# Kernel tuning notes

Measured on AMD Instinct MI355X. Metric: run time of the kernel, lower is better.

## Reference

```python
import jax, jax.numpy as jnp
import numpy as np

N, FDIM, HDIM, STEPS = 8192, 512, 1024, 50
STRESS, QNOISE = 0.0, 0.1


def setup_inputs() -> dict:
    key = jax.random.key(0)
    ks = jax.random.split(key, 20)
    s = 0.02
    d = {
        "real_antigen": jax.random.normal(ks[0], (N, FDIM), jnp.float32),
        "steps": STEPS,
        # quantum gene projection (self-loop graph -> per-node linear)
        "Wq": jax.random.normal(ks[1], (FDIM, HDIM), jnp.float32) * s,
        "bq": jnp.zeros((HDIM,), jnp.float32),
        # denoise_0: Linear(h,h) ReLU Linear(h,f)
        "W01": jax.random.normal(ks[2], (HDIM, HDIM), jnp.float32) * s,
        "b01": jnp.zeros((HDIM,), jnp.float32),
        "W02": jax.random.normal(ks[3], (HDIM, FDIM), jnp.float32) * s,
        "b02": jnp.zeros((FDIM,), jnp.float32),
        # denoise_1: Linear(h,h) Tanh Linear(h,f)
        "W11": jax.random.normal(ks[4], (HDIM, HDIM), jnp.float32) * s,
        "b11": jnp.zeros((HDIM,), jnp.float32),
        "W12": jax.random.normal(ks[5], (HDIM, FDIM), jnp.float32) * s,
        "b12": jnp.zeros((FDIM,), jnp.float32),
        # interference_net: Linear(2f,h) GELU Linear(h,f)
        "Wi1": jax.random.normal(ks[6], (2 * FDIM, HDIM), jnp.float32) * s,
        "bi1": jnp.zeros((HDIM,), jnp.float32),
        "Wi2": jax.random.normal(ks[7], (HDIM, FDIM), jnp.float32) * s,
        "bi2": jnp.zeros((FDIM,), jnp.float32),
        # quantum state scalars
        "alpha_amp": jnp.asarray(np.cos(0.6), jnp.float32),
        "beta_amp": jnp.asarray(np.sin(0.6), jnp.float32),
        "phase_cos": jnp.asarray(np.cos(0.3), jnp.float32),
    }
    return d


def reference(real_antigen, steps, Wq, bq, W01, b01, W02, b02, W11, b11,
              W12, b12, Wi1, bi1, Wi2, bi2, alpha_amp, beta_amp, phase_cos):
    sched = jnp.linspace(1e-4, 0.02, 100, dtype=jnp.float32)
    decoherence_rate = jnp.float32(0.1 + STRESS * 0.5)
    decay = jnp.exp(-decoherence_rate)
    # quantum probabilities (fixed amplitudes during the rollout)
    a2, b2 = alpha_amp ** 2, beta_amp ** 2
    p0 = a2 / (a2 + b2)
    p1 = b2 / (a2 + b2)
    sp0, sp1 = jnp.sqrt(p0), jnp.sqrt(p1)
    base_key = jax.random.key(1)
    x0 = jax.random.normal(jax.random.fold_in(base_key, 10_000), real_antigen.shape, jnp.float32)

    def step(carry, t):
        x, coh = carry
        qf = jax.nn.relu(x @ Wq + bq)                           # [N, H]
        d0 = jax.nn.relu(qf @ W01 + b01) @ W02 + b02            # [N, F]
        d1 = jnp.tanh(qf @ W11 + b11) @ W12 + b12               # [N, F]
        inter_in = jnp.concatenate([d0, d1], axis=-1)           # [N, 2F]
        interf = jax.nn.gelu(inter_in @ Wi1 + bi1, approximate=False) @ Wi2 + bi2
        qi = 2.0 * jnp.sqrt(p0 * p1) * phase_cos * coh          # scalar interference
        denoised = sp0 * d0 + sp1 * d1 + qi * interf
        alpha = jnp.maximum(1.0 - sched[t], 1e-8)
        alpha_prev = jnp.where(t > 0, 1.0 - sched[jnp.maximum(t - 1, 0)], 1.0)
        sqrt_1ma = jnp.sqrt(jnp.maximum(1.0 - alpha, 1e-8))
        x_new = (x - (1.0 - alpha) / sqrt_1ma * denoised) / jnp.sqrt(alpha)
        sigma = jnp.sqrt(jnp.maximum((1.0 - alpha_prev) / (1.0 - alpha) * (1.0 - alpha / alpha_prev), 0.0))
        noise = jax.random.normal(jax.random.fold_in(base_key, t), x.shape, jnp.float32)
        x_new = jnp.where(t > 0, x_new + (sigma + QNOISE * jnp.abs(qi)) * noise, x_new)
        return (x_new, coh * decay), None

    ts = jnp.arange(int(steps) - 1, -1, -1, dtype=jnp.int32)
    (x, _), _ = jax.lax.scan(step, (x0, jnp.float32(1.0)), ts)
    # quantum measurement: collapse to |0> with probability p0
    u = jax.random.uniform(jax.random.fold_in(base_key, 99_999), (), jnp.float32)
    dream = jnp.where(u < p0, 0.7 * x + 0.3 * real_antigen, x)
    return dream
```

## Files before the change

kernel.cpp:

```cpp
#include <hip/hip_runtime.h>
#include <stdint.h>
#include <math.h>


typedef __bf16 bf16x8 __attribute__((ext_vector_type(8)));
typedef float floatx4 __attribute__((ext_vector_type(4)));

__host__ __device__ inline void tf2x32(uint32_t k0, uint32_t k1,
                                       uint32_t x0, uint32_t x1,
                                       uint32_t& o0, uint32_t& o1) {
  uint32_t ks2 = k0 ^ k1 ^ 0x1BD11BDAu;
#define TF_R(r) { x0 += x1; x1 = (x1 << (r)) | (x1 >> (32 - (r))); x1 ^= x0; }
  x0 += k0; x1 += k1;
  TF_R(13) TF_R(15) TF_R(26) TF_R(6)
  x0 += k1;  x1 += ks2 + 1u;
  TF_R(17) TF_R(29) TF_R(16) TF_R(24)
  x0 += ks2; x1 += k0 + 2u;
  TF_R(13) TF_R(15) TF_R(26) TF_R(6)
  x0 += k0;  x1 += k1 + 3u;
  TF_R(17) TF_R(29) TF_R(16) TF_R(24)
  x0 += k1;  x1 += ks2 + 4u;
  TF_R(13) TF_R(15) TF_R(26) TF_R(6)
  x0 += ks2; x1 += k0 + 5u;
#undef TF_R
  o0 = x0; o1 = x1;
}

__device__ inline float erfinv_f32(float x) {
  float w = -log1pf(-x * x);
  float p;
  if (w < 5.0f) {
    w = w - 2.5f;
    p = 2.81022636e-08f;
    p = fmaf(p, w, 3.43273939e-07f);
    p = fmaf(p, w, -3.5233877e-06f);
    p = fmaf(p, w, -4.39150654e-06f);
    p = fmaf(p, w, 0.00021858087f);
    p = fmaf(p, w, -0.00125372503f);
    p = fmaf(p, w, -0.00417768164f);
    p = fmaf(p, w, 0.246640727f);
    p = fmaf(p, w, 1.50140941f);
  } else {
    w = sqrtf(w) - 3.0f;
    p = -0.000200214257f;
    p = fmaf(p, w, 0.000100950558f);
    p = fmaf(p, w, 0.00134934322f);
    p = fmaf(p, w, -0.00367342844f);
    p = fmaf(p, w, 0.00573950773f);
    p = fmaf(p, w, -0.0076224613f);
    p = fmaf(p, w, 0.00943887047f);
    p = fmaf(p, w, 1.00167406f);
    p = fmaf(p, w, 2.83297682f);
  }
  return p * x;
}

__device__ inline float tf_normal(uint32_t k0, uint32_t k1, uint32_t i) {
  uint32_t o0, o1;
  tf2x32(k0, k1, 0u, i, o0, o1);
  uint32_t bits = o0 ^ o1;
  float f = __uint_as_float(0x3F800000u | (bits >> 9)) - 1.0f;
  float u = f * 2.0f + (-0.99999994f);
  u = fmaxf(-0.99999994f, u);
  return 1.41421356f * erfinv_f32(u);
}

__device__ inline unsigned short f2bf(float f) {
  uint32_t u = __float_as_uint(f);
  u += 0x7FFFu + ((u >> 16) & 1u);
  return (unsigned short)(u >> 16);
}
__device__ inline float bf2f(unsigned short h) {
  return __uint_as_float(((uint32_t)h) << 16);
}

__global__ __launch_bounds__(256)
void transpose_bf16_kernel(const float* __restrict__ W,
                           unsigned short* __restrict__ Wt, int K, int N) {
  __shared__ float tile[32][33];
  int kb = blockIdx.x * 32, nb = blockIdx.y * 32;
  int tx = threadIdx.x & 31, ty = threadIdx.x >> 5;
#pragma unroll
  for (int i = 0; i < 32; i += 8)
    tile[ty + i][tx] = W[(size_t)(kb + ty + i) * N + nb + tx];
  __syncthreads();
#pragma unroll
  for (int i = 0; i < 32; i += 8)
    Wt[(size_t)(nb + ty + i) * K + kb + tx] = f2bf(tile[tx][ty + i]);
}

__device__ __forceinline__ void gemm_core_db(
    const unsigned short* __restrict__ A0, const unsigned short* __restrict__ A1,
    int lda0, int lda1, int K0, int Ktot,
    const unsigned short* __restrict__ Bt,
    int row0, int col0,
    unsigned short (*As)[128 * 32], unsigned short (*Bs)[128 * 32],
    floatx4 (&acc)[2][4]) {
  const int tid = threadIdx.x;
  const int wave = tid >> 6, lane = tid & 63;
  const int wr = wave >> 1, wc = wave & 1;
  const int srow = tid >> 2;
  const int sgr = (tid & 3) * 8;
  const int fm = lane & 15, quad = lane >> 4;

  auto issue = [&](int kt, int buf) {
    const int k0 = kt * 32;
    const unsigned short* Ap; int kOff, lda;
    if (k0 < K0) { Ap = A0; kOff = k0; lda = lda0; }
    else         { Ap = A1; kOff = k0 - K0; lda = lda1; }
    __builtin_amdgcn_global_load_lds(
        (const __attribute__((address_space(1))) uint32_t*)
            (Ap + (size_t)(row0 + srow) * lda + kOff + sgr),
        (__attribute__((address_space(3))) uint32_t*)(&As[buf][srow * 32 + sgr]),
        16, 0, 0);
    __builtin_amdgcn_global_load_lds(
        (const __attribute__((address_space(1))) uint32_t*)
            (Bt + (size_t)(col0 + srow) * Ktot + k0 + sgr),
        (__attribute__((address_space(3))) uint32_t*)(&Bs[buf][srow * 32 + sgr]),
        16, 0, 0);
  };

  const int nk = Ktot >> 5;
  issue(0, 0);
  for (int k = 0; k < nk; k++) {
    const int cur = k & 1;
    if (k + 1 < nk) {
      issue(k + 1, cur ^ 1);
      asm volatile("s_waitcnt vmcnt(2)\ns_barrier" ::: "memory");
    } else {
      asm volatile("s_waitcnt vmcnt(0)\ns_barrier" ::: "memory");
    }
    bf16x8 a[2], b[4];
#pragma unroll
    for (int tm = 0; tm < 2; tm++)
      a[tm] = *(const bf16x8*)(&As[cur][(wr * 32 + tm * 16 + fm) * 32 + quad * 8]);
#pragma unroll
    for (int tn = 0; tn < 4; tn++)
      b[tn] = *(const bf16x8*)(&Bs[cur][(wc * 64 + tn * 16 + fm) * 32 + quad * 8]);
#pragma unroll
    for (int tm = 0; tm < 2; tm++)
#pragma unroll
      for (int tn = 0; tn < 4; tn++)
        acc[tm][tn] = __builtin_amdgcn_mfma_f32_16x16x32_bf16(a[tm], b[tn],
                                                              acc[tm][tn], 0, 0, 0);
    asm volatile("s_barrier" ::: "memory");
  }
}

__device__ __forceinline__ void swizzled_block(int& row0, int& col0) {
  int id = blockIdx.x + gridDim.x * blockIdx.y;
  row0 = (id & 63) << 7;
  col0 = (id >> 6) << 7;
}

template<int ACT>
__global__ __launch_bounds__(512, 4)
void mfma_gemm(const unsigned short* __restrict__ A0,
               const unsigned short* __restrict__ A1,
               int lda0, int lda1, int K0, int Ktot,
               const unsigned short* __restrict__ Bt,
               const float* __restrict__ bias0,
               const float* __restrict__ bias1, int nsplit,
               unsigned short* __restrict__ C0,
               unsigned short* __restrict__ C1, int ldc) {
  __shared__ unsigned short As[2][128 * 32];
  __shared__ unsigned short Bs[2][128 * 32];
  int row0, col0;
  swizzled_block(row0, col0);
  floatx4 acc[2][4];
#pragma unroll
  for (int tm = 0; tm < 2; tm++)
#pragma unroll
    for (int tn = 0; tn < 4; tn++) acc[tm][tn] = (floatx4){0.f, 0.f, 0.f, 0.f};
  gemm_core_db(A0, A1, lda0, lda1, K0, Ktot, Bt, row0, col0, As, Bs, acc);

  const int lane = threadIdx.x & 63, wave = threadIdx.x >> 6;
  const int wr = wave >> 1, wc = wave & 1;
  const int fm = lane & 15, quad = lane >> 4;
  const bool side = (ACT == 4) && (col0 >= nsplit);
  const float* bias = side ? bias1 : bias0;
  unsigned short* C = side ? C1 : C0;
  const int cbase = col0 - (side ? nsplit : 0);
#pragma unroll
  for (int tn = 0; tn < 4; tn++) {
    int col = cbase + wc * 64 + tn * 16 + fm;
    float bv = bias[col];
#pragma unroll
    for (int tm = 0; tm < 2; tm++) {
      int rbase = row0 + wr * 32 + tm * 16 + quad * 4;
#pragma unroll
      for (int r = 0; r < 4; r++) {
        float val = acc[tm][tn][r] + bv;
        if (ACT == 1) val = fmaxf(val, 0.0f);
        if (ACT == 2) val = tanhf(val);
        if (ACT == 3) val = 0.5f * val * (1.0f + erff(val * 0.70710678118654752f));
        if (ACT == 4) val = side ? tanhf(val) : fmaxf(val, 0.0f);
        C[(size_t)(rbase + r) * ldc + col] = f2bf(val);
      }
    }
  }
}

__global__ __launch_bounds__(512, 4)
void mfma_gemm_pair(const unsigned short* __restrict__ Aa,
                    const unsigned short* __restrict__ Ab,
                    const unsigned short* __restrict__ Bta,
                    const unsigned short* __restrict__ Btb,
                    const float* __restrict__ biasa,
                    const float* __restrict__ biasb,
                    unsigned short* __restrict__ Ca,
                    unsigned short* __restrict__ Cb,
                    int Ktot, int ldc) {
  __shared__ unsigned short As[2][128 * 32];
  __shared__ unsigned short Bs[2][128 * 32];
  const int z = blockIdx.z;
  const unsigned short* A = z ? Ab : Aa;
  const unsigned short* Bt = z ? Btb : Bta;
  const float* bias = z ? biasb : biasa;
  unsigned short* C = z ? Cb : Ca;
  int row0, col0;
  swizzled_block(row0, col0);
  floatx4 acc[2][4];
#pragma unroll
  for (int tm = 0; tm < 2; tm++)
#pragma unroll
    for (int tn = 0; tn < 4; tn++) acc[tm][tn] = (floatx4){0.f, 0.f, 0.f, 0.f};
  gemm_core_db(A, A, Ktot, Ktot, Ktot, Ktot, Bt, row0, col0, As, Bs, acc);

  const int lane = threadIdx.x & 63, wave = threadIdx.x >> 6;
  const int wr = wave >> 1, wc = wave & 1;
  const int fm = lane & 15, quad = lane >> 4;
#pragma unroll
  for (int tn = 0; tn < 4; tn++) {
    int col = col0 + wc * 64 + tn * 16 + fm;
    float bv = bias[col];
#pragma unroll
    for (int tm = 0; tm < 2; tm++) {
      int rbase = row0 + wr * 32 + tm * 16 + quad * 4;
#pragma unroll
      for (int r = 0; r < 4; r++)
        C[(size_t)(rbase + r) * ldc + col] = f2bf(acc[tm][tn][r] + bv);
    }
  }
}

__global__ void init_normal_kernel(float* __restrict__ x,
                                   unsigned short* __restrict__ xbf,
                                   uint32_t k0, uint32_t k1, int n) {
  int i = blockIdx.x * blockDim.x + threadIdx.x;
  if (i >= n) return;
  float v = tf_normal(k0, k1, (uint32_t)i);
  x[i] = v;
  xbf[i] = f2bf(v);
}

__global__ void update_kernel(float* __restrict__ x,
                              unsigned short* __restrict__ xbf,
                              const unsigned short* __restrict__ d0,
                              const unsigned short* __restrict__ d1,
                              const unsigned short* __restrict__ itf,
                              const float* __restrict__ a_amp,
                              const float* __restrict__ b_amp,
                              const float* __restrict__ ph,
                              float coh, float c1, float sqrt_alpha,
                              float sigma, int add_noise,
                              uint32_t k0, uint32_t k1, int n) {
  int i = blockIdx.x * blockDim.x + threadIdx.x;
  if (i >= n) return;
  float aa = a_amp[0], bb = b_amp[0], pc = ph[0];
  float a2 = aa * aa, b2 = bb * bb, s = a2 + b2;
  float p0 = a2 / s, p1 = b2 / s;
  float qi = 2.0f * sqrtf(p0 * p1) * pc * coh;
  float den = sqrtf(p0) * bf2f(d0[i]) + sqrtf(p1) * bf2f(d1[i])
            + qi * bf2f(itf[i]);
  float xn = (x[i] - c1 * den) / sqrt_alpha;
  if (add_noise) {
    float nz = tf_normal(k0, k1, (uint32_t)i);
    xn += (sigma + 0.1f * fabsf(qi)) * nz;
  }
  x[i] = xn;
  xbf[i] = f2bf(xn);
}

__global__ void final_kernel(const float* __restrict__ x,
                             const float* __restrict__ real,
                             float* __restrict__ out,
                             const float* __restrict__ a_amp,
                             const float* __restrict__ b_amp,
                             uint32_t k0, uint32_t k1, int n) {
  int i = blockIdx.x * blockDim.x + threadIdx.x;
  if (i >= n) return;
  float aa = a_amp[0], bb = b_amp[0];
  float a2 = aa * aa, b2 = bb * bb;
  float p0 = a2 / (a2 + b2);
  uint32_t o0, o1;
  tf2x32(k0, k1, 0u, 0u, o0, o1);
  uint32_t bits = o0 ^ o1;
  float u = __uint_as_float(0x3F800000u | (bits >> 9)) - 1.0f;
  float xv = x[i];
  out[i] = (u < p0) ? (0.7f * xv + 0.3f * real[i]) : xv;
}

extern "C" void kernel_launch(void* const* d_in, const int* in_sizes, int n_in,
                              void* d_out, int out_size, void* d_ws,
                              size_t ws_size, hipStream_t stream) {
  const float* real = (const float*)d_in[0];
  const float* Wq  = (const float*)d_in[2];
  const float* bq  = (const float*)d_in[3];
  const float* W01 = (const float*)d_in[4];
  const float* b01 = (const float*)d_in[5];
  const float* W02 = (const float*)d_in[6];
  const float* b02 = (const float*)d_in[7];
  const float* W11 = (const float*)d_in[8];
  const float* b11 = (const float*)d_in[9];
  const float* W12 = (const float*)d_in[10];
  const float* b12 = (const float*)d_in[11];
  const float* Wi1 = (const float*)d_in[12];
  const float* bi1 = (const float*)d_in[13];
  const float* Wi2 = (const float*)d_in[14];
  const float* bi2 = (const float*)d_in[15];
  const float* a_amp = (const float*)d_in[16];
  const float* b_amp = (const float*)d_in[17];
  const float* ph    = (const float*)d_in[18];

  const int Nn = 8192, F = 512, H = 1024;
  const int nElem = Nn * F;
  const int NSPLIT_OFF = 1 << 30;

  char* ws = (char*)d_ws;
  float* x = (float*)ws;                                   ws += (size_t)nElem * 4;
  unsigned short* xbf = (unsigned short*)ws;               ws += (size_t)nElem * 2;
  unsigned short* qf  = (unsigned short*)ws;               ws += (size_t)Nn * H * 2;
  unsigned short* h0  = (unsigned short*)ws;               ws += (size_t)Nn * H * 2;
  unsigned short* h1  = (unsigned short*)ws;               ws += (size_t)Nn * H * 2;
  unsigned short* d0  = (unsigned short*)ws;               ws += (size_t)nElem * 2;
  unsigned short* d1  = (unsigned short*)ws;               ws += (size_t)nElem * 2;
  unsigned short* itf = (unsigned short*)ws;               ws += (size_t)nElem * 2;
  unsigned short* Wq_t  = (unsigned short*)ws;             ws += (size_t)F * H * 2;
  unsigned short* WA_t  = (unsigned short*)ws;             ws += (size_t)(2 * H) * H * 2;
  unsigned short* W02_t = (unsigned short*)ws;             ws += (size_t)H * F * 2;
  unsigned short* W12_t = (unsigned short*)ws;             ws += (size_t)H * F * 2;
  unsigned short* Wi1_t = (unsigned short*)ws;             ws += (size_t)(2 * F) * H * 2;
  unsigned short* Wi2_t = (unsigned short*)ws;             ws += (size_t)H * F * 2;

  dim3 tb(256);
  transpose_bf16_kernel<<<dim3(F / 32, H / 32), tb, 0, stream>>>(Wq, Wq_t, F, H);
  transpose_bf16_kernel<<<dim3(H / 32, H / 32), tb, 0, stream>>>(W01, WA_t, H, H);
  transpose_bf16_kernel<<<dim3(H / 32, H / 32), tb, 0, stream>>>(W11, WA_t + (size_t)H * H, H, H);
  transpose_bf16_kernel<<<dim3(H / 32, F / 32), tb, 0, stream>>>(W02, W02_t, H, F);
  transpose_bf16_kernel<<<dim3(H / 32, F / 32), tb, 0, stream>>>(W12, W12_t, H, F);
  transpose_bf16_kernel<<<dim3(2 * F / 32, H / 32), tb, 0, stream>>>(Wi1, Wi1_t, 2 * F, H);
  transpose_bf16_kernel<<<dim3(H / 32, F / 32), tb, 0, stream>>>(Wi2, Wi2_t, H, F);

  uint32_t kx0, kx1; tf2x32(0u, 1u, 0u, 10000u, kx0, kx1);
  init_normal_kernel<<<(nElem + 255) / 256, 256, 0, stream>>>(x, xbf, kx0, kx1, nElem);

  float sched[100];
  for (int i = 0; i < 100; i++)
    sched[i] = (float)(1e-4 + (0.02 - 1e-4) * (double)i / 99.0);
  const float decay = expf(-0.1f);
  float coh = 1.0f;

  dim3 blk(512);
  dim3 g1(H / 128, 64);
  dim3 g2(2 * H / 128, 64);
  dim3 g45(F / 128, 64, 2);
  dim3 g6(H / 128, 64);
  dim3 g7(F / 128, 64);

  for (int j = 0; j < 50; j++) {
    int t = 49 - j;
    mfma_gemm<1><<<g1, blk, 0, stream>>>(xbf, xbf, F, F, F, F, Wq_t,
                                         bq, nullptr, NSPLIT_OFF, qf, nullptr, H);
    mfma_gemm<4><<<g2, blk, 0, stream>>>(qf, qf, H, H, H, H, WA_t,
                                         b01, b11, H, h0, h1, H);
    mfma_gemm_pair<<<g45, blk, 0, stream>>>(h0, h1, W02_t, W12_t, b02, b12,
                                            d0, d1, H, F);
    mfma_gemm<3><<<g6, blk, 0, stream>>>(d0, d1, F, F, F, 2 * F, Wi1_t,
                                         bi1, nullptr, NSPLIT_OFF, qf, nullptr, H);
    mfma_gemm<0><<<g7, blk, 0, stream>>>(qf, qf, H, H, H, H, Wi2_t,
                                         bi2, nullptr, NSPLIT_OFF, itf, nullptr, F);

    float schedt = sched[t];
    float alphaf = fmaxf(1.0f - schedt, 1e-8f);
    float one_m_alpha = 1.0f - alphaf;
    float sqrt_1ma = sqrtf(fmaxf(one_m_alpha, 1e-8f));
    float c1 = one_m_alpha / sqrt_1ma;
    float sqa = sqrtf(alphaf);
    float sigma = 0.0f;
    if (t > 0) {
      float ap = 1.0f - sched[t - 1];
      sigma = sqrtf(fmaxf((1.0f - ap) / one_m_alpha * (1.0f - alphaf / ap), 0.0f));
    }
    uint32_t kt0, kt1; tf2x32(0u, 1u, 0u, (uint32_t)t, kt0, kt1);
    update_kernel<<<(nElem + 255) / 256, 256, 0, stream>>>(
        x, xbf, d0, d1, itf, a_amp, b_amp, ph, coh, c1, sqa, sigma,
        (t > 0) ? 1 : 0, kt0, kt1, nElem);
    coh *= decay;
  }

  uint32_t ku0, ku1; tf2x32(0u, 1u, 0u, 99999u, ku0, ku1);
  final_kernel<<<(nElem + 255) / 256, 256, 0, stream>>>(
      x, real, (float*)d_out, a_amp, b_amp, ku0, ku1, nElem);
}
```

Baseline: 8.881 ms.

## Fuse interference output GEMM with diffusion update epilogue

Replaces the final Wi2 GEMM plus the separate elementwise update kernel with one MFMA GEMM whose epilogue computes the denoised combination, the noise and the x update directly. This drops the bf16 itf intermediate buffer and one kernel launch per step, saving a write and read of N*F values. The new GEMM uses a smaller 64x128 tile with 8 waves, each doing 2x2 MFMA tiles, and loads into LDS asynchronously via global_load_lds with double buffering. That tiling may lower MFMA efficiency compared with the previous generic GEMM, and the epilogue's scattered per-element loads of x, d0 and d1 may coalesce less well.

```diff
diff --git a/kernel.cpp b/kernel.cpp
--- a/kernel.cpp
+++ b/kernel.cpp
@@ -244,6 +244,107 @@
   }
 }
 
+__global__ __launch_bounds__(512, 4)
+void mfma_gemm_update(const unsigned short* __restrict__ A,
+                      const unsigned short* __restrict__ Bt,
+                      const float* __restrict__ bias,
+                      const unsigned short* __restrict__ d0,
+                      const unsigned short* __restrict__ d1,
+                      float* __restrict__ x,
+                      unsigned short* __restrict__ xbf,
+                      const float* __restrict__ a_amp,
+                      const float* __restrict__ b_amp,
+                      const float* __restrict__ ph,
+                      float coh, float c1, float sqa, float sigma,
+                      int add_noise, uint32_t k0, uint32_t k1) {
+  __shared__ unsigned short As[2][64 * 32];
+  __shared__ unsigned short Bs[2][128 * 32];
+  const int tid = threadIdx.x;
+  const int wave = tid >> 6, lane = tid & 63;
+  const int wr = wave >> 2, wc = wave & 3;
+  const int fm = lane & 15, quad = lane >> 4;
+  const int id = blockIdx.x + gridDim.x * blockIdx.y;
+  const int row0 = (id & 127) << 6;
+  const int col0 = (id >> 7) << 7;
+  const int sArow = (tid & 255) >> 2;
+  const int sBrow = tid >> 2;
+  const int sgr = (tid & 3) * 8;
+
+  auto issue = [&](int kt, int buf) {
+    const int kk = kt * 32;
+    __builtin_amdgcn_global_load_lds(
+        (const __attribute__((address_space(1))) uint32_t*)
+            (A + (size_t)(row0 + sArow) * 1024 + kk + sgr),
+        (__attribute__((address_space(3))) uint32_t*)(&As[buf][sArow * 32 + sgr]),
+        16, 0, 0);
+    __builtin_amdgcn_global_load_lds(
+        (const __attribute__((address_space(1))) uint32_t*)
+            (Bt + (size_t)(col0 + sBrow) * 1024 + kk + sgr),
+        (__attribute__((address_space(3))) uint32_t*)(&Bs[buf][sBrow * 32 + sgr]),
+        16, 0, 0);
+  };
+
+  floatx4 acc[2][2];
+#pragma unroll
+  for (int tm = 0; tm < 2; tm++)
+#pragma unroll
+    for (int tn = 0; tn < 2; tn++) acc[tm][tn] = (floatx4){0.f, 0.f, 0.f, 0.f};
+
+  const int nk = 32;
+  issue(0, 0);
+  for (int k = 0; k < nk; k++) {
+    const int cur = k & 1;
+    if (k + 1 < nk) {
+      issue(k + 1, cur ^ 1);
+      asm volatile("s_waitcnt vmcnt(2)\ns_barrier" ::: "memory");
+    } else {
+      asm volatile("s_waitcnt vmcnt(0)\ns_barrier" ::: "memory");
+    }
+    bf16x8 a[2], b[2];
+#pragma unroll
+    for (int tm = 0; tm < 2; tm++)
+      a[tm] = *(const bf16x8*)(&As[cur][(wr * 32 + tm * 16 + fm) * 32 + quad * 8]);
+#pragma unroll
+    for (int tn = 0; tn < 2; tn++)
+      b[tn] = *(const bf16x8*)(&Bs[cur][(wc * 32 + tn * 16 + fm) * 32 + quad * 8]);
+#pragma unroll
+    for (int tm = 0; tm < 2; tm++)
+#pragma unroll
+      for (int tn = 0; tn < 2; tn++)
+        acc[tm][tn] = __builtin_amdgcn_mfma_f32_16x16x32_bf16(a[tm], b[tn],
+                                                              acc[tm][tn], 0, 0, 0);
+    asm volatile("s_barrier" ::: "memory");
+  }
+
+  float aa = a_amp[0], bb = b_amp[0], pc = ph[0];
+  float a2 = aa * aa, b2 = bb * bb, s = a2 + b2;
+  float p0 = a2 / s, p1 = b2 / s;
+  float sp0 = sqrtf(p0), sp1 = sqrtf(p1);
+  float qi = 2.0f * sqrtf(p0 * p1) * pc * coh;
+  float nscale = sigma + 0.1f * fabsf(qi);
+
+#pragma unroll
+  for (int tn = 0; tn < 2; tn++) {
+    int col = col0 + wc * 32 + tn * 16 + fm;
+    float bv = bias[col];
+#pragma unroll
+    for (int tm = 0; tm < 2; tm++) {
+      int rbase = row0 + wr * 32 + tm * 16 + quad * 4;
+#pragma unroll
+      for (int r = 0; r < 4; r++) {
+        int row = rbase + r;
+        size_t i = (size_t)row * 512 + col;
+        float itf = acc[tm][tn][r] + bv;
+        float den = sp0 * bf2f(d0[i]) + sp1 * bf2f(d1[i]) + qi * itf;
+        float xn = (x[i] - c1 * den) / sqa;
+        if (add_noise) xn += nscale * tf_normal(k0, k1, (uint32_t)i);
+        x[i] = xn;
+        xbf[i] = f2bf(xn);
+      }
+    }
+  }
+}
+
 __global__ void init_normal_kernel(float* __restrict__ x,
                                    unsigned short* __restrict__ xbf,
                                    uint32_t k0, uint32_t k1, int n) {
@@ -252,34 +353,6 @@
   float v = tf_normal(k0, k1, (uint32_t)i);
   x[i] = v;
   xbf[i] = f2bf(v);
-}
-
-__global__ void update_kernel(float* __restrict__ x,
-                              unsigned short* __restrict__ xbf,
-                              const unsigned short* __restrict__ d0,
-                              const unsigned short* __restrict__ d1,
-                              const unsigned short* __restrict__ itf,
-                              const float* __restrict__ a_amp,
-                              const float* __restrict__ b_amp,
-                              const float* __restrict__ ph,
-                              float coh, float c1, float sqrt_alpha,
-                              float sigma, int add_noise,
-                              uint32_t k0, uint32_t k1, int n) {
-  int i = blockIdx.x * blockDim.x + threadIdx.x;
-  if (i >= n) return;
-  float aa = a_amp[0], bb = b_amp[0], pc = ph[0];
-  float a2 = aa * aa, b2 = bb * bb, s = a2 + b2;
-  float p0 = a2 / s, p1 = b2 / s;
-  float qi = 2.0f * sqrtf(p0 * p1) * pc * coh;
-  float den = sqrtf(p0) * bf2f(d0[i]) + sqrtf(p1) * bf2f(d1[i])
-            + qi * bf2f(itf[i]);
-  float xn = (x[i] - c1 * den) / sqrt_alpha;
-  if (add_noise) {
-    float nz = tf_normal(k0, k1, (uint32_t)i);
-    xn += (sigma + 0.1f * fabsf(qi)) * nz;
-  }
-  x[i] = xn;
-  xbf[i] = f2bf(xn);
 }
 
 __global__ void final_kernel(const float* __restrict__ x,
@@ -335,7 +408,6 @@
   unsigned short* h1  = (unsigned short*)ws;               ws += (size_t)Nn * H * 2;
   unsigned short* d0  = (unsigned short*)ws;               ws += (size_t)nElem * 2;
   unsigned short* d1  = (unsigned short*)ws;               ws += (size_t)nElem * 2;
-  unsigned short* itf = (unsigned short*)ws;               ws += (size_t)nElem * 2;
   unsigned short* Wq_t  = (unsigned short*)ws;             ws += (size_t)F * H * 2;
   unsigned short* WA_t  = (unsigned short*)ws;             ws += (size_t)(2 * H) * H * 2;
   unsigned short* W02_t = (unsigned short*)ws;             ws += (size_t)H * F * 2;
@@ -366,7 +438,7 @@
   dim3 g2(2 * H / 128, 64);
   dim3 g45(F / 128, 64, 2);
   dim3 g6(H / 128, 64);
-  dim3 g7(F / 128, 64);
+  dim3 g7(F / 128, Nn / 64);
 
   for (int j = 0; j < 50; j++) {
     int t = 49 - j;
@@ -378,8 +450,6 @@
                                             d0, d1, H, F);
     mfma_gemm<3><<<g6, blk, 0, stream>>>(d0, d1, F, F, F, 2 * F, Wi1_t,
                                          bi1, nullptr, NSPLIT_OFF, qf, nullptr, H);
-    mfma_gemm<0><<<g7, blk, 0, stream>>>(qf, qf, H, H, H, H, Wi2_t,
-                                         bi2, nullptr, NSPLIT_OFF, itf, nullptr, F);
 
     float schedt = sched[t];
     float alphaf = fmaxf(1.0f - schedt, 1e-8f);
@@ -393,9 +463,9 @@
       sigma = sqrtf(fmaxf((1.0f - ap) / one_m_alpha * (1.0f - alphaf / ap), 0.0f));
     }
     uint32_t kt0, kt1; tf2x32(0u, 1u, 0u, (uint32_t)t, kt0, kt1);
-    update_kernel<<<(nElem + 255) / 256, 256, 0, stream>>>(
-        x, xbf, d0, d1, itf, a_amp, b_amp, ph, coh, c1, sqa, sigma,
-        (t > 0) ? 1 : 0, kt0, kt1, nElem);
+    mfma_gemm_update<<<g7, blk, 0, stream>>>(
+        qf, Wi2_t, bi2, d0, d1, x, xbf, a_amp, b_amp, ph, coh, c1, sqa, sigma,
+        (t > 0) ? 1 : 0, kt0, kt1);
     coh *= decay;
   }
 
```

Result: faster. 8.392 ms (-5.5%).
